# Optimization experiments

Measured on AMD Instinct MI355X. Metric: run time of the kernel, lower is better.

Reference implementation:

```python
import jax, jax.numpy as jnp
import numpy as np

LENGTHSCALES = np.array([0.1, 0.2, 0.5, 1.0, 2.0, 5.0, 10.0, 20.0], dtype=np.float32)
VALUE_DIM = 64
OUTPUT_DIM = 512
NUM_HEADS = len(LENGTHSCALES)


def setup_inputs() -> dict:
    key = jax.random.key(0)
    k1, k2, k3, k4, k5 = jax.random.split(key, 5)
    B, Lq, Lk, D = 4, 2048, 2048, 3
    query_positions = jax.random.normal(k1, (B, Lq, D), dtype=jnp.float32)
    key_positions = jax.random.normal(k2, (B, Lk, D), dtype=jnp.float32)
    values = jax.random.normal(k3, (B, Lk, NUM_HEADS, VALUE_DIM), dtype=jnp.float32)
    masked_elements = jax.random.randint(k4, (B, Lk), 0, 2) > 0
    # nn.Linear(value_dim*num_heads, output_dim, bias=False): weight [out, in]
    fan_in = VALUE_DIM * NUM_HEADS
    w_out = jax.random.uniform(k5, (OUTPUT_DIM, fan_in), dtype=jnp.float32,
                               minval=-1.0, maxval=1.0) / jnp.sqrt(fan_in)
    lengthscales = jnp.asarray(LENGTHSCALES)
    return {"query_positions": query_positions, "key_positions": key_positions,
            "values": values, "masked_elements": masked_elements,
            "lengthscales": lengthscales, "w_out": w_out}


def reference(query_positions, key_positions, values, masked_elements, lengthscales, w_out):
    # Euclidean distances via mm-trick (matches torch.cdist use_mm_for_euclid_dist)
    q2 = jnp.sum(query_positions ** 2, axis=-1)            # [B, Lq]
    k2 = jnp.sum(key_positions ** 2, axis=-1)              # [B, Lk]
    qk = jnp.einsum('bqd,bkd->bqk', query_positions, key_positions)
    d2 = jnp.maximum(q2[:, :, None] + k2[:, None, :] - 2.0 * qk, 0.0)
    distances = jnp.sqrt(d2)                               # [B, Lq, Lk]
    # per-head scaling + gaussian basis: exp(-(d/ls)^2)
    scaled = distances[:, None, :, :] / lengthscales[None, :, None, None]  # [B, H, Lq, Lk]
    scores = jnp.exp(-(scaled ** 2))
    scores = jnp.where(masked_elements[:, None, None, :], 0.0, scores)
    # masked sum-normalization
    scores = scores / (jnp.sum(jnp.abs(scores), axis=-1, keepdims=True) + 1e-5)
    # attend: values [B, Lk, H, V] -> [B, H, Lk, V]; then flatten heads -> [B, Lq, H*V]
    attended = jnp.einsum('bhqk,bkhv->bqhv', scores, values)
    B, Lq = attended.shape[0], attended.shape[1]
    flat = attended.reshape(B, Lq, -1)
    return flat @ w_out.T                                   # [B, Lq, output_dim]
```

## Files before the change

### kernel.cpp

```cpp
#include <hip/hip_runtime.h>
#include <math.h>

#define BB 4
#define LQ 2048
#define LK 2048
#define HD 8
#define VD 64
#define HV 512
#define SP 72

typedef __attribute__((ext_vector_type(8))) short bf16x8;
typedef __attribute__((ext_vector_type(4))) float f32x4;

static __device__ __forceinline__ unsigned short f2bf(float f) {
    unsigned u = __builtin_bit_cast(unsigned, f);
    unsigned r = (u + 0x7fffu + ((u >> 16) & 1u)) >> 16;
    return (unsigned short)r;
}

static __device__ __forceinline__ float fast_exp2(float x) {
#if __has_builtin(__builtin_amdgcn_exp2f)
    return __builtin_amdgcn_exp2f(x);
#else
    return __expf(x * 0.69314718f);
#endif
}

static __device__ __forceinline__ unsigned pack_trunc(float even, float odd) {
    return __builtin_amdgcn_perm(__builtin_bit_cast(unsigned, odd),
                                 __builtin_bit_cast(unsigned, even), 0x07060302u);
}

__global__ __launch_bounds__(256) void cvt_vals(
    const float* __restrict__ vals, unsigned short* __restrict__ vals_t)
{
    __shared__ unsigned short st[64 * SP];
    const int tid = threadIdx.x;
    const int kt = blockIdx.x, h = blockIdx.y, b = blockIdx.z;

    const int k  = tid >> 2;
    const int vb = (tid & 3) * 16;
    const float* src = vals + (((size_t)(b * LK + kt * 64 + k) * HD + h)) * VD + vb;
    float4 f0 = *(const float4*)(src);
    float4 f1 = *(const float4*)(src + 4);
    float4 f2 = *(const float4*)(src + 8);
    float4 f3 = *(const float4*)(src + 12);
    const float fv[16] = {f0.x,f0.y,f0.z,f0.w, f1.x,f1.y,f1.z,f1.w,
                          f2.x,f2.y,f2.z,f2.w, f3.x,f3.y,f3.z,f3.w};
#pragma unroll
    for (int j = 0; j < 16; ++j) st[(vb + j) * SP + k] = f2bf(fv[j]);
    __syncthreads();

    const int v  = tid >> 2;
    const int kb = (tid & 3) * 16;
    uint4 o0 = *(const uint4*)&st[v * SP + kb];
    uint4 o1 = *(const uint4*)&st[v * SP + kb + 8];
    unsigned short* dst = vals_t + ((size_t)((b * HD + h) * VD + v)) * LK + kt * 64 + kb;
    *(uint4*)dst       = o0;
    *(uint4*)(dst + 8) = o1;
}

__global__ __launch_bounds__(256) void cvt_w(
    const float* __restrict__ w, unsigned short* __restrict__ wb)
{
    const int i = (blockIdx.x * 256 + threadIdx.x) * 4;
    float4 f = *(const float4*)(w + i);
    ushort4 o;
    o.x = f2bf(f.x); o.y = f2bf(f.y); o.z = f2bf(f.z); o.w = f2bf(f.w);
    *(ushort4*)(wb + i) = o;
}

__global__ __launch_bounds__(256) void attend4(
    const float* __restrict__ qpos,
    const float* __restrict__ kpos,
    const unsigned short* __restrict__ vals_t,
    const int*   __restrict__ kmask,
    const float* __restrict__ ls,
    unsigned short* __restrict__ attended)
{
    const int tid = threadIdx.x;
    const int bi  = blockIdx.x;
    const int xcd = bi & 7, sub = (bi >> 3) & 3, qc = bi >> 5;
    const int slice = xcd * 4 + sub;
    const int b = slice >> 3, h = slice & 7;
    const int wave = tid >> 6, lane = tid & 63;
    const int ln = lane & 15, kq = lane >> 4;

    const float lsh = ls[h];
    const float ch  = -1.44269504f / (lsh * lsh);

    const int qbase = qc * 128 + wave * 32;
    float qx[2], qy[2], qz[2];
#pragma unroll
    for (int st = 0; st < 2; ++st) {
        const float* qp = qpos + (size_t)(b * LQ + qbase + st * 16 + ln) * 3;
        qx[st] = qp[0]; qy[st] = qp[1]; qz[st] = qp[2];
    }

    const unsigned short* vbase = vals_t + (size_t)((b * HD + h) * VD) * LK;
    const float* kpb = kpos + (size_t)b * LK * 3;
    const int*   kmb = kmask + b * LK;

    f32x4 acc[2][4];
#pragma unroll
    for (int i = 0; i < 2; ++i)
#pragma unroll
        for (int j = 0; j < 4; ++j) acc[i][j] = (f32x4){0.f, 0.f, 0.f, 0.f};
    float pden[2] = {0.f, 0.f};

    for (int t = 0; t < 32; ++t) {
        bf16x8 bf0[4], bf1[4];
#pragma unroll
        for (int vt = 0; vt < 4; ++vt) {
            const unsigned short* bp = vbase + (size_t)(vt * 16 + ln) * LK + t * 64 + kq * 8;
            bf0[vt] = *(const bf16x8*)(bp);
            bf1[vt] = *(const bf16x8*)(bp + 32);
        }

        bf16x8 afr[2][2];
#pragma unroll
        for (int half = 0; half < 2; ++half) {
            const int K0 = t * 64 + half * 32 + kq * 8;
            float4 kc[6];
            const float* ksrc = kpb + (size_t)K0 * 3;
#pragma unroll
            for (int j = 0; j < 6; ++j) kc[j] = ((const float4*)ksrc)[j];
            int mk[8];
            *(int4*)&mk[0] = *(const int4*)(kmb + K0);
            *(int4*)&mk[4] = *(const int4*)(kmb + K0 + 4);
            const float* kcf = (const float*)kc;
            float xs[8], ys[8], zs[8];
#pragma unroll
            for (int j = 0; j < 8; ++j) {
                xs[j] = mk[j] ? 3.0e37f : kcf[3 * j];
                ys[j] = kcf[3 * j + 1];
                zs[j] = kcf[3 * j + 2];
            }
#pragma unroll
            for (int st = 0; st < 2; ++st) {
                float s[8];
#pragma unroll
                for (int j = 0; j < 8; ++j) {
                    const float dx = qx[st] - xs[j];
                    const float dy = qy[st] - ys[j];
                    const float dz = qz[st] - zs[j];
                    const float d2 = fmaf(dx, dx, fmaf(dy, dy, dz * dz));
                    const float sc = fast_exp2(d2 * ch);
                    pden[st] += sc;
                    s[j] = sc;
                }
                unsigned pk[4];
#pragma unroll
                for (int p = 0; p < 4; ++p) pk[p] = pack_trunc(s[2 * p], s[2 * p + 1]);
                afr[st][half] = __builtin_bit_cast(bf16x8, *(uint4*)pk);
            }
        }

#pragma unroll
        for (int st = 0; st < 2; ++st)
#pragma unroll
            for (int vt = 0; vt < 4; ++vt) {
                acc[st][vt] = __builtin_amdgcn_mfma_f32_16x16x32_bf16(afr[st][0], bf0[vt], acc[st][vt], 0, 0, 0);
                acc[st][vt] = __builtin_amdgcn_mfma_f32_16x16x32_bf16(afr[st][1], bf1[vt], acc[st][vt], 0, 0, 0);
            }
    }

    float inv[2];
#pragma unroll
    for (int st = 0; st < 2; ++st) {
        float v = pden[st];
        v += __shfl_xor(v, 16, 64);
        v += __shfl_xor(v, 32, 64);
        inv[st] = 1.0f / (v + 1e-5f);
    }
    float ivq[2][4];
#pragma unroll
    for (int st = 0; st < 2; ++st)
#pragma unroll
        for (int r = 0; r < 4; ++r) ivq[st][r] = __shfl(inv[st], kq * 4 + r, 64);

#pragma unroll
    for (int st = 0; st < 2; ++st)
#pragma unroll
        for (int vt = 0; vt < 4; ++vt)
#pragma unroll
            for (int r = 0; r < 4; ++r) {
                const int q = qbase + st * 16 + kq * 4 + r;
                attended[(size_t)(b * LQ + q) * HV + h * VD + vt * 16 + ln] =
                    f2bf(acc[st][vt][r] * ivq[st][r]);
            }
}

__global__ __launch_bounds__(256, 1) void proj4(
    const unsigned short* __restrict__ A,
    const unsigned short* __restrict__ Wb,
    float* __restrict__ C)
{
    __shared__ __align__(16) unsigned short sA[128 * SP];
    __shared__ __align__(16) unsigned short sW[128 * SP];

    const int tid = threadIdx.x;
    const int n0 = blockIdx.x * 128, m0 = blockIdx.y * 128;
    const int wave = tid >> 6, lane = tid & 63;
    const int ln = lane & 15, kq = lane >> 4;
    const int mw = (wave >> 1) * 64, nw = (wave & 1) * 64;
    const int sr = tid >> 1, sh = (tid & 1) * 32;

    f32x4 acc[4][4];
#pragma unroll
    for (int i = 0; i < 4; ++i)
#pragma unroll
        for (int j = 0; j < 4; ++j) acc[i][j] = (f32x4){0.f, 0.f, 0.f, 0.f};

    for (int k0 = 0; k0 < 512; k0 += 64) {
        __syncthreads();
        {
            const unsigned short* a = A  + (size_t)(m0 + sr) * 512 + k0 + sh;
            const unsigned short* w = Wb + (size_t)(n0 + sr) * 512 + k0 + sh;
            uint4 a0 = ((const uint4*)a)[0], a1 = ((const uint4*)a)[1],
                  a2 = ((const uint4*)a)[2], a3 = ((const uint4*)a)[3];
            uint4 w0 = ((const uint4*)w)[0], w1 = ((const uint4*)w)[1],
                  w2 = ((const uint4*)w)[2], w3 = ((const uint4*)w)[3];
            unsigned short* da = &sA[sr * SP + sh];
            unsigned short* dw = &sW[sr * SP + sh];
            ((uint4*)da)[0] = a0; ((uint4*)da)[1] = a1;
            *(uint4*)(da + 16) = a2; *(uint4*)(da + 24) = a3;
            ((uint4*)dw)[0] = w0; ((uint4*)dw)[1] = w1;
            *(uint4*)(dw + 16) = w2; *(uint4*)(dw + 24) = w3;
        }
        __syncthreads();

        bf16x8 af[4][2], bfr[4][2];
#pragma unroll
        for (int mt = 0; mt < 4; ++mt) {
            const unsigned short* ap = &sA[(mw + mt * 16 + ln) * SP + kq * 8];
            af[mt][0] = *(const bf16x8*)(ap);
            af[mt][1] = *(const bf16x8*)(ap + 32);
        }
#pragma unroll
        for (int nt = 0; nt < 4; ++nt) {
            const unsigned short* bp = &sW[(nw + nt * 16 + ln) * SP + kq * 8];
            bfr[nt][0] = *(const bf16x8*)(bp);
            bfr[nt][1] = *(const bf16x8*)(bp + 32);
        }
#pragma unroll
        for (int mt = 0; mt < 4; ++mt)
#pragma unroll
            for (int nt = 0; nt < 4; ++nt) {
                acc[mt][nt] = __builtin_amdgcn_mfma_f32_16x16x32_bf16(af[mt][0], bfr[nt][0], acc[mt][nt], 0, 0, 0);
                acc[mt][nt] = __builtin_amdgcn_mfma_f32_16x16x32_bf16(af[mt][1], bfr[nt][1], acc[mt][nt], 0, 0, 0);
            }
    }

#pragma unroll
    for (int mt = 0; mt < 4; ++mt)
#pragma unroll
        for (int nt = 0; nt < 4; ++nt)
#pragma unroll
            for (int r = 0; r < 4; ++r)
                C[(size_t)(m0 + mw + mt * 16 + kq * 4 + r) * 512 + n0 + nw + nt * 16 + ln] =
                    acc[mt][nt][r];
}

extern "C" void kernel_launch(void* const* d_in, const int* in_sizes, int n_in,
                              void* d_out, int out_size, void* d_ws, size_t ws_size,
                              hipStream_t stream) {
    const float* qpos  = (const float*)d_in[0];
    const float* kpos  = (const float*)d_in[1];
    const float* vals  = (const float*)d_in[2];
    const int*   kmask = (const int*)  d_in[3];
    const float* ls    = (const float*)d_in[4];
    const float* wout  = (const float*)d_in[5];
    float* out = (float*)d_out;

    unsigned short* vals_t   = (unsigned short*)d_ws;
    unsigned short* attended = vals_t + (size_t)4 * 1024 * 1024;
    unsigned short* w_bf     = vals_t + (size_t)8 * 1024 * 1024;

    cvt_vals<<<dim3(32, HD, BB), 256, 0, stream>>>(vals, vals_t);
    cvt_w   <<<dim3(256), 256, 0, stream>>>(wout, w_bf);
    attend4 <<<dim3(512), 256, 0, stream>>>(qpos, kpos, vals_t, kmask, ls, attended);
    proj4   <<<dim3(4, 64), 256, 0, stream>>>(attended, w_bf, out);
}
```

Measured before the change: 194.0 us.

## Prescale key positions per head, double-buffer attend loads, shrink projection tiles

```diff
diff --git a/kernel.cpp b/kernel.cpp
--- a/kernel.cpp
+++ b/kernel.cpp
@@ -8,6 +8,8 @@
 #define VD 64
 #define HV 512
 #define SP 72
+
+#define COORD_SCALE 1.2011224087864498f
 
 typedef __attribute__((ext_vector_type(8))) short bf16x8;
 typedef __attribute__((ext_vector_type(4))) float f32x4;
@@ -70,11 +72,23 @@
     *(ushort4*)(wb + i) = o;
 }
 
-__global__ __launch_bounds__(256) void attend4(
+__global__ __launch_bounds__(256) void bake_kpos(
+    const float* __restrict__ kpos, const int* __restrict__ kmask,
+    const float* __restrict__ ls, float* __restrict__ kposm)
+{
+    const int i = blockIdx.x * 256 + threadIdx.x;
+    const int h = i >> 13, bk = i & 8191;
+    const float s = COORD_SCALE / ls[h];
+    float x = kpos[3 * bk] * s, y = kpos[3 * bk + 1] * s, z = kpos[3 * bk + 2] * s;
+    if (kmask[bk]) x = 1.0e38f;
+    float* d = kposm + ((size_t)h * BB * LK + bk) * 3;
+    d[0] = x; d[1] = y; d[2] = z;
+}
+
+__global__ __launch_bounds__(256) void attend5(
     const float* __restrict__ qpos,
-    const float* __restrict__ kpos,
+    const float* __restrict__ kposm,
     const unsigned short* __restrict__ vals_t,
-    const int*   __restrict__ kmask,
     const float* __restrict__ ls,
     unsigned short* __restrict__ attended)
 {
@@ -86,20 +100,31 @@
     const int wave = tid >> 6, lane = tid & 63;
     const int ln = lane & 15, kq = lane >> 4;
 
-    const float lsh = ls[h];
-    const float ch  = -1.44269504f / (lsh * lsh);
+    const float sh = COORD_SCALE / ls[h];
 
     const int qbase = qc * 128 + wave * 32;
     float qx[2], qy[2], qz[2];
 #pragma unroll
     for (int st = 0; st < 2; ++st) {
         const float* qp = qpos + (size_t)(b * LQ + qbase + st * 16 + ln) * 3;
-        qx[st] = qp[0]; qy[st] = qp[1]; qz[st] = qp[2];
+        qx[st] = qp[0] * sh; qy[st] = qp[1] * sh; qz[st] = qp[2] * sh;
     }
 
     const unsigned short* vbase = vals_t + (size_t)((b * HD + h) * VD) * LK;
-    const float* kpb = kpos + (size_t)b * LK * 3;
-    const int*   kmb = kmask + b * LK;
+    const uint4* pB[4];
+#pragma unroll
+    for (int vt = 0; vt < 4; ++vt)
+        pB[vt] = (const uint4*)(vbase + (size_t)(vt * 16 + ln) * LK + kq * 8);
+    const float4* pC = (const float4*)(kposm + ((size_t)h * BB * LK + (size_t)b * LK + kq * 8) * 3);
+
+    uint4  bB[2][8];
+    float4 bC[2][12];
+
+#pragma unroll
+    for (int vt = 0; vt < 4; ++vt) { bB[0][2*vt] = pB[vt][0]; bB[0][2*vt+1] = pB[vt][4]; pB[vt] += 8; }
+#pragma unroll
+    for (int j = 0; j < 6; ++j) { bC[0][j] = pC[j]; bC[0][6+j] = pC[24+j]; }
+    pC += 48;
 
     f32x4 acc[2][4];
 #pragma unroll
@@ -108,44 +133,37 @@
         for (int j = 0; j < 4; ++j) acc[i][j] = (f32x4){0.f, 0.f, 0.f, 0.f};
     float pden[2] = {0.f, 0.f};
 
+#pragma unroll 2
     for (int t = 0; t < 32; ++t) {
-        bf16x8 bf0[4], bf1[4];
-#pragma unroll
-        for (int vt = 0; vt < 4; ++vt) {
-            const unsigned short* bp = vbase + (size_t)(vt * 16 + ln) * LK + t * 64 + kq * 8;
-            bf0[vt] = *(const bf16x8*)(bp);
-            bf1[vt] = *(const bf16x8*)(bp + 32);
-        }
-
+        const int cur = t & 1, nxt = cur ^ 1;
+
+        if (t < 31) {
+#pragma unroll
+            for (int vt = 0; vt < 4; ++vt) {
+                bB[nxt][2*vt]   = pB[vt][0];
+                bB[nxt][2*vt+1] = pB[vt][4];
+                pB[vt] += 8;
+            }
+#pragma unroll
+            for (int j = 0; j < 6; ++j) { bC[nxt][j] = pC[j]; bC[nxt][6+j] = pC[24+j]; }
+            pC += 48;
+        }
+
+        const float* kcf = (const float*)&bC[cur][0];
         bf16x8 afr[2][2];
 #pragma unroll
         for (int half = 0; half < 2; ++half) {
-            const int K0 = t * 64 + half * 32 + kq * 8;
-            float4 kc[6];
-            const float* ksrc = kpb + (size_t)K0 * 3;
-#pragma unroll
-            for (int j = 0; j < 6; ++j) kc[j] = ((const float4*)ksrc)[j];
-            int mk[8];
-            *(int4*)&mk[0] = *(const int4*)(kmb + K0);
-            *(int4*)&mk[4] = *(const int4*)(kmb + K0 + 4);
-            const float* kcf = (const float*)kc;
-            float xs[8], ys[8], zs[8];
-#pragma unroll
-            for (int j = 0; j < 8; ++j) {
-                xs[j] = mk[j] ? 3.0e37f : kcf[3 * j];
-                ys[j] = kcf[3 * j + 1];
-                zs[j] = kcf[3 * j + 2];
-            }
+            const float* kc = kcf + half * 24;
 #pragma unroll
             for (int st = 0; st < 2; ++st) {
                 float s[8];
 #pragma unroll
                 for (int j = 0; j < 8; ++j) {
-                    const float dx = qx[st] - xs[j];
-                    const float dy = qy[st] - ys[j];
-                    const float dz = qz[st] - zs[j];
+                    const float dx = qx[st] - kc[3 * j];
+                    const float dy = qy[st] - kc[3 * j + 1];
+                    const float dz = qz[st] - kc[3 * j + 2];
                     const float d2 = fmaf(dx, dx, fmaf(dy, dy, dz * dz));
-                    const float sc = fast_exp2(d2 * ch);
+                    const float sc = fast_exp2(-d2);
                     pden[st] += sc;
                     s[j] = sc;
                 }
@@ -160,8 +178,10 @@
         for (int st = 0; st < 2; ++st)
 #pragma unroll
             for (int vt = 0; vt < 4; ++vt) {
-                acc[st][vt] = __builtin_amdgcn_mfma_f32_16x16x32_bf16(afr[st][0], bf0[vt], acc[st][vt], 0, 0, 0);
-                acc[st][vt] = __builtin_amdgcn_mfma_f32_16x16x32_bf16(afr[st][1], bf1[vt], acc[st][vt], 0, 0, 0);
+                const bf16x8 b0 = __builtin_bit_cast(bf16x8, *(uint4*)&bB[cur][2*vt]);
+                const bf16x8 b1 = __builtin_bit_cast(bf16x8, *(uint4*)&bB[cur][2*vt+1]);
+                acc[st][vt] = __builtin_amdgcn_mfma_f32_16x16x32_bf16(afr[st][0], b0, acc[st][vt], 0, 0, 0);
+                acc[st][vt] = __builtin_amdgcn_mfma_f32_16x16x32_bf16(afr[st][1], b1, acc[st][vt], 0, 0, 0);
             }
     }
 
@@ -191,71 +211,67 @@
             }
 }
 
-__global__ __launch_bounds__(256, 1) void proj4(
+__global__ __launch_bounds__(256, 4) void proj5(
     const unsigned short* __restrict__ A,
     const unsigned short* __restrict__ Wb,
     float* __restrict__ C)
 {
-    __shared__ __align__(16) unsigned short sA[128 * SP];
-    __shared__ __align__(16) unsigned short sW[128 * SP];
+    __shared__ __align__(16) unsigned short sA[64 * SP];
+    __shared__ __align__(16) unsigned short sW[64 * SP];
 
     const int tid = threadIdx.x;
-    const int n0 = blockIdx.x * 128, m0 = blockIdx.y * 128;
+    const int n0 = blockIdx.x * 64, m0 = blockIdx.y * 64;
     const int wave = tid >> 6, lane = tid & 63;
     const int ln = lane & 15, kq = lane >> 4;
-    const int mw = (wave >> 1) * 64, nw = (wave & 1) * 64;
-    const int sr = tid >> 1, sh = (tid & 1) * 32;
-
-    f32x4 acc[4][4];
-#pragma unroll
-    for (int i = 0; i < 4; ++i)
-#pragma unroll
-        for (int j = 0; j < 4; ++j) acc[i][j] = (f32x4){0.f, 0.f, 0.f, 0.f};
+    const int mw = (wave >> 1) * 32, nw = (wave & 1) * 32;
+    const int srow = tid >> 2, skb = (tid & 3) * 16;
+
+    f32x4 acc[2][2];
+#pragma unroll
+    for (int i = 0; i < 2; ++i)
+#pragma unroll
+        for (int j = 0; j < 2; ++j) acc[i][j] = (f32x4){0.f, 0.f, 0.f, 0.f};
 
     for (int k0 = 0; k0 < 512; k0 += 64) {
         __syncthreads();
         {
-            const unsigned short* a = A  + (size_t)(m0 + sr) * 512 + k0 + sh;
-            const unsigned short* w = Wb + (size_t)(n0 + sr) * 512 + k0 + sh;
-            uint4 a0 = ((const uint4*)a)[0], a1 = ((const uint4*)a)[1],
-                  a2 = ((const uint4*)a)[2], a3 = ((const uint4*)a)[3];
-            uint4 w0 = ((const uint4*)w)[0], w1 = ((const uint4*)w)[1],
-                  w2 = ((const uint4*)w)[2], w3 = ((const uint4*)w)[3];
-            unsigned short* da = &sA[sr * SP + sh];
-            unsigned short* dw = &sW[sr * SP + sh];
+            const unsigned short* a = A  + (size_t)(m0 + srow) * 512 + k0 + skb;
+            const unsigned short* w = Wb + (size_t)(n0 + srow) * 512 + k0 + skb;
+            uint4 a0 = ((const uint4*)a)[0], a1 = ((const uint4*)a)[1];
+            uint4 w0 = ((const uint4*)w)[0], w1 = ((const uint4*)w)[1];
+            unsigned short* da = &sA[srow * SP + skb];
+            unsigned short* dw = &sW[srow * SP + skb];
             ((uint4*)da)[0] = a0; ((uint4*)da)[1] = a1;
-            *(uint4*)(da + 16) = a2; *(uint4*)(da + 24) = a3;
             ((uint4*)dw)[0] = w0; ((uint4*)dw)[1] = w1;
-            *(uint4*)(dw + 16) = w2; *(uint4*)(dw + 24) = w3;
         }
         __syncthreads();
 
-        bf16x8 af[4][2], bfr[4][2];
-#pragma unroll
-        for (int mt = 0; mt < 4; ++mt) {
+        bf16x8 af[2][2], bfr[2][2];
+#pragma unroll
+        for (int mt = 0; mt < 2; ++mt) {
             const unsigned short* ap = &sA[(mw + mt * 16 + ln) * SP + kq * 8];
             af[mt][0] = *(const bf16x8*)(ap);
             af[mt][1] = *(const bf16x8*)(ap + 32);
         }
 #pragma unroll
-        for (int nt = 0; nt < 4; ++nt) {
+        for (int nt = 0; nt < 2; ++nt) {
             const unsigned short* bp = &sW[(nw + nt * 16 + ln) * SP + kq * 8];
             bfr[nt][0] = *(const bf16x8*)(bp);
             bfr[nt][1] = *(const bf16x8*)(bp + 32);
         }
 #pragma unroll
-        for (int mt = 0; mt < 4; ++mt)
-#pragma unroll
-            for (int nt = 0; nt < 4; ++nt) {
+        for (int mt = 0; mt < 2; ++mt)
+#pragma unroll
+            for (int nt = 0; nt < 2; ++nt) {
                 acc[mt][nt] = __builtin_amdgcn_mfma_f32_16x16x32_bf16(af[mt][0], bfr[nt][0], acc[mt][nt], 0, 0, 0);
                 acc[mt][nt] = __builtin_amdgcn_mfma_f32_16x16x32_bf16(af[mt][1], bfr[nt][1], acc[mt][nt], 0, 0, 0);
             }
     }
 
 #pragma unroll
-    for (int mt = 0; mt < 4; ++mt)
-#pragma unroll
-        for (int nt = 0; nt < 4; ++nt)
+    for (int mt = 0; mt < 2; ++mt)
+#pragma unroll
+        for (int nt = 0; nt < 2; ++nt)
 #pragma unroll
             for (int r = 0; r < 4; ++r)
                 C[(size_t)(m0 + mw + mt * 16 + kq * 4 + r) * 512 + n0 + nw + nt * 16 + ln] =
@@ -276,9 +292,11 @@
     unsigned short* vals_t   = (unsigned short*)d_ws;
     unsigned short* attended = vals_t + (size_t)4 * 1024 * 1024;
     unsigned short* w_bf     = vals_t + (size_t)8 * 1024 * 1024;
-
-    cvt_vals<<<dim3(32, HD, BB), 256, 0, stream>>>(vals, vals_t);
-    cvt_w   <<<dim3(256), 256, 0, stream>>>(wout, w_bf);
-    attend4 <<<dim3(512), 256, 0, stream>>>(qpos, kpos, vals_t, kmask, ls, attended);
-    proj4   <<<dim3(4, 64), 256, 0, stream>>>(attended, w_bf, out);
-}
+    float*          kposm    = (float*)(vals_t + (size_t)8 * 1024 * 1024 + 512 * 1024);
+
+    cvt_vals <<<dim3(32, HD, BB), 256, 0, stream>>>(vals, vals_t);
+    cvt_w    <<<dim3(256), 256, 0, stream>>>(wout, w_bf);
+    bake_kpos<<<dim3(HD * BB * LK / 256), 256, 0, stream>>>(kpos, kmask, ls, kposm);
+    attend5  <<<dim3(512), 256, 0, stream>>>(qpos, kposm, vals_t, ls, attended);
+    proj5    <<<dim3(512 / 64, (BB * LQ) / 64), 256, 0, stream>>>(attended, w_bf, out);
+}
```

Result: slower. 200.5 us (+3.4%).
